# Performance work log

Hardware: AMD Instinct MI355X
Metric: run time of the kernel (lower is better)

## Reference

```python
import jax, jax.numpy as jnp
import numpy as np

N = 100000
E = 3200000
IN_F = 256
OUT_F = 256
CLAMP = 10.0


def setup_inputs() -> dict:
    key = jax.random.key(0)
    k1, k2, k3, k4, k5 = jax.random.split(key, 5)
    x = jax.random.normal(k1, (N, IN_F), dtype=jnp.float32)
    adj_rows = jnp.sort(jax.random.randint(k2, (E,), 0, N, dtype=jnp.int32))
    adj_cols = jax.random.randint(k3, (E,), 0, N, dtype=jnp.int32)
    adj_vals = jax.random.uniform(k4, (E,), dtype=jnp.float32)
    # glorot-ish init (scaled by 0.1 as in the module)
    stdv = 0.1 * np.sqrt(6.0 / (IN_F + OUT_F))
    weight = jax.random.uniform(k5, (IN_F, OUT_F), dtype=jnp.float32,
                                minval=-stdv, maxval=stdv)
    bias = jnp.zeros((OUT_F,), dtype=jnp.float32)
    return {"x": x, "adj_rows": adj_rows, "adj_cols": adj_cols,
            "adj_vals": adj_vals, "weight": weight, "bias": bias}


def reference(x, adj_rows, adj_cols, adj_vals, weight, bias):
    # clamp input
    x = jnp.clip(x, -CLAMP, CLAMP)
    # dense projection: [N, in] @ [in, out]
    support = jnp.clip(x @ weight, -CLAMP, CLAMP)
    # sparse adjacency SpMM: out[r] += val * support[c] for each edge (r, c)
    msgs = adj_vals[:, None] * support[adj_cols]          # [E, out]
    output = jax.ops.segment_sum(msgs, adj_rows, num_segments=N)
    output = jnp.clip(output, -CLAMP, CLAMP)
    output = output + bias
    output = jax.nn.relu(output)
    return jnp.clip(output, -CLAMP, CLAMP)
```

## Files before the change

### kernel.cpp

```cpp
#include <hip/hip_runtime.h>

#define N_NODES 100000
#define N_EDGES 3200000
#define IN_F    256
#define OUT_F   256
#define CLAMP_V 10.0f

typedef __attribute__((ext_vector_type(8))) short bf16x8;
typedef __attribute__((ext_vector_type(4))) float f32x4;

__device__ __forceinline__ float clampf(float v) {
    return fminf(fmaxf(v, -CLAMP_V), CLAMP_V);
}
__device__ __forceinline__ unsigned f2bf(float f) {
    unsigned u = __float_as_uint(f);
    u += 0x7fffu + ((u >> 16) & 1u);
    return u >> 16;
}
__device__ __forceinline__ unsigned cvt_pk_bf16(float lo, float hi) {
    unsigned r;
    asm("v_cvt_pk_bf16_f32 %0, %1, %2" : "=v"(r) : "v"(lo), "v"(hi));
    return r;
}
__device__ __forceinline__ float bflo(unsigned w) { return __uint_as_float(w << 16); }
__device__ __forceinline__ float bfhi(unsigned w) { return __uint_as_float(w & 0xffff0000u); }

__global__ __launch_bounds__(256) void convert_w(
    const float* __restrict__ w, unsigned short* __restrict__ wt) {
    int i = blockIdx.x * 256 + threadIdx.x;
    int k = i & 255, n = i >> 8;
    float v = w[(size_t)k * OUT_F + n];
    int dst = ((k >> 3) << 11) + (n << 3) + (k & 7);
    wt[dst] = (unsigned short)f2bf(v);
}

__global__ __launch_bounds__(256) void build_row_ptr(
    const int* __restrict__ rows, int* __restrict__ row_ptr) {
    int r = blockIdx.x * blockDim.x + threadIdx.x;
    if (r > N_NODES) return;
    int lo = 0, hi = N_EDGES;
    while (lo < hi) {
        int mid = (lo + hi) >> 1;
        if (rows[mid] < r) lo = mid + 1; else hi = mid;
    }
    row_ptr[r] = lo;
}

__global__ __launch_bounds__(256) void gemm_mfma(
    const float* __restrict__ x, const unsigned short* __restrict__ wt,
    unsigned* __restrict__ sup8, float* __restrict__ scales) {
    __shared__ char sl[32768];

    const int t    = threadIdx.x;
    const int lane = t & 63;
    const int wc   = t >> 6;
    const int l15  = lane & 15;
    const int l4   = lane >> 4;
    const int blockRow = blockIdx.x * 64;

    const float* aptr[4];
    #pragma unroll
    for (int m = 0; m < 4; ++m) {
        int r = blockRow + m * 16 + l15;
        aptr[m] = x + (size_t)(r < N_NODES ? r : N_NODES - 1) * IN_F + l4 * 8;
    }
    const unsigned short* bptr = wt + (l4 << 11) + ((wc * 64 + l15) << 3);

    f32x4 acc[4][4];
    #pragma unroll
    for (int m = 0; m < 4; ++m)
        #pragma unroll
        for (int n = 0; n < 4; ++n)
            acc[m][n] = (f32x4)0.f;

    #pragma unroll
    for (int s = 0; s < 8; ++s) {
        bf16x8 a[4], b[4];
        #pragma unroll
        for (int m = 0; m < 4; ++m) {
            float4 u0 = *(const float4*)(aptr[m] + s * 32);
            float4 u1 = *(const float4*)(aptr[m] + s * 32 + 4);
            union { unsigned u[4]; bf16x8 v; } pk;
            pk.u[0] = cvt_pk_bf16(clampf(u0.x), clampf(u0.y));
            pk.u[1] = cvt_pk_bf16(clampf(u0.z), clampf(u0.w));
            pk.u[2] = cvt_pk_bf16(clampf(u1.x), clampf(u1.y));
            pk.u[3] = cvt_pk_bf16(clampf(u1.z), clampf(u1.w));
            a[m] = pk.v;
        }
        #pragma unroll
        for (int n = 0; n < 4; ++n)
            b[n] = *(const bf16x8*)(bptr + (s << 13) + (n << 7));
        #pragma unroll
        for (int m = 0; m < 4; ++m)
            #pragma unroll
            for (int n = 0; n < 4; ++n)
                acc[m][n] = __builtin_amdgcn_mfma_f32_16x16x32_bf16(
                    a[m], b[n], acc[m][n], 0, 0, 0);
    }

    #pragma unroll
    for (int m = 0; m < 4; ++m) {
        #pragma unroll
        for (int n = 0; n < 4; ++n) {
            int col2 = (wc * 64 + n * 16 + l15) * 2;
            #pragma unroll
            for (int r = 0; r < 4; ++r) {
                int row = m * 16 + l4 * 4 + r;
                int off = row * 512 + (col2 ^ (((row >> 2) & 3) << 4));
                *(unsigned short*)(sl + off) = (unsigned short)f2bf(clampf(acc[m][n][r]));
            }
        }
    }
    __syncthreads();

    {
        const uint4* sl4 = (const uint4*)sl;
        const int row = t >> 2;
        const int qt  = t & 3;
        const int swz = (row >> 2) & 3;

        uint4 c[8];
        float mx = 0.f;
        #pragma unroll
        for (int j = 0; j < 8; ++j) {
            c[j] = sl4[row * 32 + ((qt * 8 + j) ^ swz)];
            const unsigned* cu = (const unsigned*)&c[j];
            #pragma unroll
            for (int q = 0; q < 4; ++q)
                mx = fmaxf(mx, fmaxf(fabsf(bflo(cu[q])), fabsf(bfhi(cu[q]))));
        }
        mx = fmaxf(mx, __shfl_xor(mx, 1));
        mx = fmaxf(mx, __shfl_xor(mx, 2));

        const float inv = 127.f / fmaxf(mx, 1e-30f);
        const int grow = blockRow + row;
        if (grow < N_NODES) {
            unsigned p[16];
            #pragma unroll
            for (int j = 0; j < 8; ++j) {
                const unsigned* cu = (const unsigned*)&c[j];
                #pragma unroll
                for (int q = 0; q < 2; ++q) {
                    unsigned b0 = (unsigned)(int)rintf(bflo(cu[q*2+0]) * inv) + 128u;
                    unsigned b1 = (unsigned)(int)rintf(bfhi(cu[q*2+0]) * inv) + 128u;
                    unsigned b2 = (unsigned)(int)rintf(bflo(cu[q*2+1]) * inv) + 128u;
                    unsigned b3 = (unsigned)(int)rintf(bfhi(cu[q*2+1]) * inv) + 128u;
                    p[j*2+q] = b0 | (b1 << 8) | (b2 << 16) | (b3 << 24);
                }
            }
            uint4* dst = (uint4*)(sup8 + (size_t)grow * 64 + qt * 16);
            #pragma unroll
            for (int j = 0; j < 4; ++j)
                dst[j] = *(const uint4*)&p[j * 4];
            if (qt == 0) scales[grow] = mx * (1.f / 127.f);
        }
    }
}

#define FMAQ(g, vs)                                                       \
    S += (vs);                                                            \
    acc[0] += (vs) * (float)((g).x & 0xffu);                              \
    acc[1] += (vs) * (float)(((g).x >> 8) & 0xffu);                       \
    acc[2] += (vs) * (float)(((g).x >> 16) & 0xffu);                      \
    acc[3] += (vs) * (float)((g).x >> 24);                                \
    acc[4] += (vs) * (float)((g).y & 0xffu);                              \
    acc[5] += (vs) * (float)(((g).y >> 8) & 0xffu);                       \
    acc[6] += (vs) * (float)(((g).y >> 16) & 0xffu);                      \
    acc[7] += (vs) * (float)((g).y >> 24);

__global__ __launch_bounds__(256) void spmm_out(
    const unsigned* __restrict__ sup8, const float* __restrict__ scales,
    const int* __restrict__ row_ptr, const int* __restrict__ cols,
    const float* __restrict__ vals, const float* __restrict__ bias,
    float* __restrict__ out) {
    const int wid  = threadIdx.x >> 6;
    const int lane = threadIdx.x & 63;
    const int row  = blockIdx.x * 4 + wid;
    if (row >= N_NODES) return;

    const int e0   = row_ptr[row];
    const int e1   = row_ptr[row + 1];
    const int half = lane >> 5;
    const int c32  = lane & 31;

    const uint2* sup2 = (const uint2*)sup8;
    float acc[8] = {0.f,0.f,0.f,0.f,0.f,0.f,0.f,0.f};
    float S = 0.f;

    int e = e0;
    for (; e + 8 <= e1; e += 8) {
        int   ea = e + half, eb = ea + 2, ec = ea + 4, ed = ea + 6;
        int   ca = cols[ea], cb = cols[eb], cc = cols[ec], cd = cols[ed];
        float va = vals[ea], vb = vals[eb], vc = vals[ec], vd = vals[ed];
        float vsa = va * scales[ca], vsb = vb * scales[cb];
        float vsc = vc * scales[cc], vsd = vd * scales[cd];
        uint2 ga = sup2[(size_t)ca * 32 + c32];
        uint2 gb = sup2[(size_t)cb * 32 + c32];
        uint2 gc = sup2[(size_t)cc * 32 + c32];
        uint2 gd = sup2[(size_t)cd * 32 + c32];
        FMAQ(ga, vsa); FMAQ(gb, vsb); FMAQ(gc, vsc); FMAQ(gd, vsd);
    }
    for (; e + 4 <= e1; e += 4) {
        int   ea = e + half, eb = ea + 2;
        int   ca = cols[ea], cb = cols[eb];
        float va = vals[ea], vb = vals[eb];
        float vsa = va * scales[ca], vsb = vb * scales[cb];
        uint2 ga = sup2[(size_t)ca * 32 + c32];
        uint2 gb = sup2[(size_t)cb * 32 + c32];
        FMAQ(ga, vsa); FMAQ(gb, vsb);
    }
    for (; e < e1; e += 2) {
        int   ea = e + half;
        bool  ok = ea < e1;
        int   ca = cols[ok ? ea : e];
        float va = ok ? vals[ea] : 0.f;
        float vsa = va * scales[ca];
        uint2 ga = sup2[(size_t)ca * 32 + c32];
        FMAQ(ga, vsa);
    }

    S *= 128.f;
    #pragma unroll
    for (int j = 0; j < 8; ++j)
        acc[j] -= S;

    #pragma unroll
    for (int j = 0; j < 8; ++j)
        acc[j] += __shfl_xor(acc[j], 32);

    const float4 b4 = ((const float4*)bias)[c32 * 2 + half];
    f32x4 o;
    o.x = fminf(fmaxf(clampf(acc[half * 4 + 0]) + b4.x, 0.f), CLAMP_V);
    o.y = fminf(fmaxf(clampf(acc[half * 4 + 1]) + b4.y, 0.f), CLAMP_V);
    o.z = fminf(fmaxf(clampf(acc[half * 4 + 2]) + b4.z, 0.f), CLAMP_V);
    o.w = fminf(fmaxf(clampf(acc[half * 4 + 3]) + b4.w, 0.f), CLAMP_V);
    __builtin_nontemporal_store(o, (f32x4*)(out + (size_t)row * OUT_F + c32 * 8 + half * 4));
}

extern "C" void kernel_launch(void* const* d_in, const int* in_sizes, int n_in,
                              void* d_out, int out_size, void* d_ws, size_t ws_size,
                              hipStream_t stream) {
    const float* x        = (const float*)d_in[0];
    const int*   adj_rows = (const int*)d_in[1];
    const int*   adj_cols = (const int*)d_in[2];
    const float* adj_vals = (const float*)d_in[3];
    const float* weight   = (const float*)d_in[4];
    const float* bias     = (const float*)d_in[5];
    float*       out      = (float*)d_out;

    char* ws = (char*)d_ws;
    unsigned*       sup8    = (unsigned*)ws;
    float*          scales  = (float*)(ws + 25600000);
    int*            row_ptr = (int*)(ws + 26000000);
    unsigned short* wt      = (unsigned short*)(ws + 26400064);

    convert_w<<<256, 256, 0, stream>>>(weight, wt);
    build_row_ptr<<<(N_NODES + 1 + 255) / 256, 256, 0, stream>>>(adj_rows, row_ptr);
    gemm_mfma<<<(N_NODES + 63) / 64, 256, 0, stream>>>(x, wt, sup8, scales);
    spmm_out<<<(N_NODES + 3) / 4, 256, 0, stream>>>(sup8, scales, row_ptr,
                                                    adj_cols, adj_vals, bias, out);
}
```

Before: 200.3 us.

## Stage x tiles through double-buffered LDS with coalesced loads; merge prep kernels

The GEMM kernel now loads x rows with coalesced 64-byte-per-thread global reads into an XOR-swizzled, double-buffered LDS tile and prefetches the next K-slice into registers while computing. A-fragments for MFMA are then read from LDS instead of strided global loads. Weight conversion and row_ptr construction are merged into a single launch to remove one kernel launch. This adds LDS traffic and a barrier per K-step in exchange for better global-load coalescing.

```diff
diff --git a/kernel.cpp b/kernel.cpp
--- a/kernel.cpp
+++ b/kernel.cpp
@@ -25,31 +25,32 @@
 __device__ __forceinline__ float bflo(unsigned w) { return __uint_as_float(w << 16); }
 __device__ __forceinline__ float bfhi(unsigned w) { return __uint_as_float(w & 0xffff0000u); }
 
-__global__ __launch_bounds__(256) void convert_w(
-    const float* __restrict__ w, unsigned short* __restrict__ wt) {
-    int i = blockIdx.x * 256 + threadIdx.x;
-    int k = i & 255, n = i >> 8;
-    float v = w[(size_t)k * OUT_F + n];
-    int dst = ((k >> 3) << 11) + (n << 3) + (k & 7);
-    wt[dst] = (unsigned short)f2bf(v);
-}
-
-__global__ __launch_bounds__(256) void build_row_ptr(
+__global__ __launch_bounds__(256) void prep(
+    const float* __restrict__ w, unsigned short* __restrict__ wt,
     const int* __restrict__ rows, int* __restrict__ row_ptr) {
-    int r = blockIdx.x * blockDim.x + threadIdx.x;
-    if (r > N_NODES) return;
-    int lo = 0, hi = N_EDGES;
-    while (lo < hi) {
-        int mid = (lo + hi) >> 1;
-        if (rows[mid] < r) lo = mid + 1; else hi = mid;
-    }
-    row_ptr[r] = lo;
+    const int bid = blockIdx.x;
+    if (bid < 256) {
+        int i = bid * 256 + threadIdx.x;
+        int k = i & 255, n = i >> 8;
+        float v = w[(size_t)k * OUT_F + n];
+        int dst = ((k >> 3) << 11) + (n << 3) + (k & 7);
+        wt[dst] = (unsigned short)f2bf(v);
+    } else {
+        int r = (bid - 256) * 256 + threadIdx.x;
+        if (r > N_NODES) return;
+        int lo = 0, hi = N_EDGES;
+        while (lo < hi) {
+            int mid = (lo + hi) >> 1;
+            if (rows[mid] < r) lo = mid + 1; else hi = mid;
+        }
+        row_ptr[r] = lo;
+    }
 }
 
 __global__ __launch_bounds__(256) void gemm_mfma(
     const float* __restrict__ x, const unsigned short* __restrict__ wt,
     unsigned* __restrict__ sup8, float* __restrict__ scales) {
-    __shared__ char sl[32768];
+    __shared__ char lds[32768];
 
     const int t    = threadIdx.x;
     const int lane = t & 63;
@@ -58,13 +59,21 @@
     const int l4   = lane >> 4;
     const int blockRow = blockIdx.x * 64;
 
-    const float* aptr[4];
-    #pragma unroll
-    for (int m = 0; m < 4; ++m) {
-        int r = blockRow + m * 16 + l15;
-        aptr[m] = x + (size_t)(r < N_NODES ? r : N_NODES - 1) * IN_F + l4 * 8;
-    }
-    const unsigned short* bptr = wt + (l4 << 11) + ((wc * 64 + l15) << 3);
+    const int srow = t >> 2;
+    const int sqt  = t & 3;
+    int sgrow = blockRow + srow; if (sgrow >= N_NODES) sgrow = N_NODES - 1;
+    const float* sbase = x + (size_t)sgrow * IN_F + sqt * 16;
+    int woff[4];
+    #pragma unroll
+    for (int j = 0; j < 4; ++j) {
+        int chunk = sqt * 4 + j;
+        woff[j] = srow * 256 + ((chunk ^ (srow & 15)) << 4);
+    }
+
+    f32x4 st[4];
+    #pragma unroll
+    for (int j = 0; j < 4; ++j)
+        st[j] = *(const f32x4*)(sbase + j * 4);
 
     f32x4 acc[4][4];
     #pragma unroll
@@ -74,47 +83,70 @@
             acc[m][n] = (f32x4)0.f;
 
     #pragma unroll
-    for (int s = 0; s < 8; ++s) {
-        bf16x8 a[4], b[4];
+    for (int s = 0; s < 4; ++s) {
+        char* buf = lds + (s & 1) * 16384;
+        #pragma unroll
+        for (int j = 0; j < 4; ++j)
+            *(f32x4*)(buf + woff[j]) = st[j];
+        if (s < 3) {
+            const float* nb = sbase + (s + 1) * 64;
+            #pragma unroll
+            for (int j = 0; j < 4; ++j)
+                st[j] = *(const f32x4*)(nb + j * 4);
+        }
+        __syncthreads();
+
+        #pragma unroll
+        for (int kk = 0; kk < 2; ++kk) {
+            bf16x8 a[4], b[4];
+            #pragma unroll
+            for (int m = 0; m < 4; ++m) {
+                const int row = m * 16 + l15;
+                const int c0 = (kk * 8 + l4 * 2 + 0) ^ l15;
+                const int c1 = (kk * 8 + l4 * 2 + 1) ^ l15;
+                f32x4 u0 = *(const f32x4*)(buf + row * 256 + (c0 << 4));
+                f32x4 u1 = *(const f32x4*)(buf + row * 256 + (c1 << 4));
+                union { unsigned u[4]; bf16x8 v; } pk;
+                pk.u[0] = cvt_pk_bf16(clampf(u0[0]), clampf(u0[1]));
+                pk.u[1] = cvt_pk_bf16(clampf(u0[2]), clampf(u0[3]));
+                pk.u[2] = cvt_pk_bf16(clampf(u1[0]), clampf(u1[1]));
+                pk.u[3] = cvt_pk_bf16(clampf(u1[2]), clampf(u1[3]));
+                a[m] = pk.v;
+            }
+            const int kg = s * 8 + kk * 4 + l4;
+            #pragma unroll
+            for (int n = 0; n < 4; ++n)
+                b[n] = *(const bf16x8*)(wt + (kg << 11) + ((wc * 64 + n * 16 + l15) << 3));
+            #pragma unroll
+            for (int m = 0; m < 4; ++m)
+                #pragma unroll
+                for (int n = 0; n < 4; ++n)
+                    acc[m][n] = __builtin_amdgcn_mfma_f32_16x16x32_bf16(
+                        a[m], b[n], acc[m][n], 0, 0, 0);
+        }
+    }
+    __syncthreads();
+
+    {
+        char* sl = lds;
         #pragma unroll
         for (int m = 0; m < 4; ++m) {
-            float4 u0 = *(const float4*)(aptr[m] + s * 32);
-            float4 u1 = *(const float4*)(aptr[m] + s * 32 + 4);
-            union { unsigned u[4]; bf16x8 v; } pk;
-            pk.u[0] = cvt_pk_bf16(clampf(u0.x), clampf(u0.y));
-            pk.u[1] = cvt_pk_bf16(clampf(u0.z), clampf(u0.w));
-            pk.u[2] = cvt_pk_bf16(clampf(u1.x), clampf(u1.y));
-            pk.u[3] = cvt_pk_bf16(clampf(u1.z), clampf(u1.w));
-            a[m] = pk.v;
-        }
-        #pragma unroll
-        for (int n = 0; n < 4; ++n)
-            b[n] = *(const bf16x8*)(bptr + (s << 13) + (n << 7));
-        #pragma unroll
-        for (int m = 0; m < 4; ++m)
-            #pragma unroll
-            for (int n = 0; n < 4; ++n)
-                acc[m][n] = __builtin_amdgcn_mfma_f32_16x16x32_bf16(
-                    a[m], b[n], acc[m][n], 0, 0, 0);
-    }
-
-    #pragma unroll
-    for (int m = 0; m < 4; ++m) {
-        #pragma unroll
-        for (int n = 0; n < 4; ++n) {
-            int col2 = (wc * 64 + n * 16 + l15) * 2;
-            #pragma unroll
-            for (int r = 0; r < 4; ++r) {
-                int row = m * 16 + l4 * 4 + r;
-                int off = row * 512 + (col2 ^ (((row >> 2) & 3) << 4));
-                *(unsigned short*)(sl + off) = (unsigned short)f2bf(clampf(acc[m][n][r]));
+            #pragma unroll
+            for (int n = 0; n < 4; ++n) {
+                int col2 = (wc * 64 + n * 16 + l15) * 2;
+                #pragma unroll
+                for (int r = 0; r < 4; ++r) {
+                    int row = m * 16 + l4 * 4 + r;
+                    int off = row * 512 + (col2 ^ (((row >> 2) & 3) << 4));
+                    *(unsigned short*)(sl + off) = (unsigned short)f2bf(clampf(acc[m][n][r]));
+                }
             }
         }
     }
     __syncthreads();
 
     {
-        const uint4* sl4 = (const uint4*)sl;
+        const uint4* sl4 = (const uint4*)lds;
         const int row = t >> 2;
         const int qt  = t & 3;
         const int swz = (row >> 2) & 3;
@@ -254,8 +286,8 @@
     int*            row_ptr = (int*)(ws + 26000000);
     unsigned short* wt      = (unsigned short*)(ws + 26400064);
 
-    convert_w<<<256, 256, 0, stream>>>(weight, wt);
-    build_row_ptr<<<(N_NODES + 1 + 255) / 256, 256, 0, stream>>>(adj_rows, row_ptr);
+    const int rp_blocks = (N_NODES + 1 + 255) / 256;
+    prep<<<256 + rp_blocks, 256, 0, stream>>>(weight, wt, adj_rows, row_ptr);
     gemm_mfma<<<(N_NODES + 63) / 64, 256, 0, stream>>>(x, wt, sup8, scales);
     spmm_out<<<(N_NODES + 3) / 4, 256, 0, stream>>>(sup8, scales, row_ptr,
                                                     adj_cols, adj_vals, bias, out);
```

Result: faster. 174.3 us, median of 2 (-13.0%).
